# Kernel optimization log

Measured on AMD Instinct MI355X. Metric: run time of the kernel, lower is better.

The kernel has to match this reference:

```python
import jax, jax.numpy as jnp
import numpy as np

B, N, E = 2, 16384, 262144          # batch, nodes, directed edges (avg deg 16)
K, D, Wm = 256, 3, 1                # nmodes, ndims, nmeasures
C, L, FC = 128, 4, 128              # channels, Fourier layers, fc hidden
IN_DIM, OUT_DIM = 3, 1


def setup_inputs() -> dict:
    key = jax.random.key(0)
    ks = jax.random.split(key, 20)
    s = 1.0 / (C * C)
    inp = {
        "x": jax.random.normal(ks[0], (B, N, IN_DIM), jnp.float32),
        "nodes": jax.random.uniform(ks[1], (B, N, D), jnp.float32),
        "node_mask": jnp.ones((B, N, 1), jnp.float32),
        "node_weights": jax.random.uniform(ks[2], (B, N, Wm), jnp.float32) / N,
        "directed_edges": jax.random.randint(ks[3], (B, E, 2), 0, N),
        "edge_gradient_weights": jax.random.normal(ks[4], (B, E, D), jnp.float32),
        "modes": jax.random.normal(ks[5], (K, D, Wm), jnp.float32),
        "sp_L": jnp.ones((D, Wm), jnp.float32),
        "weights_c": s * jax.random.uniform(ks[6], (L, C, C, K, Wm), jnp.float32),
        "weights_s": s * jax.random.uniform(ks[7], (L, C, C, K, Wm), jnp.float32),
        "weights_0": s * jax.random.uniform(ks[8], (L, C, C, 1, Wm), jnp.float32),
        "fc0_w": jax.random.normal(ks[9], (C, IN_DIM), jnp.float32) * 0.1,
        "fc0_b": jnp.zeros((C,), jnp.float32),
        "ws_w": jax.random.normal(ks[10], (L, C, C), jnp.float32) * 0.05,
        "ws_b": jnp.zeros((L, C), jnp.float32),
        "gws_w": jax.random.normal(ks[11], (L, C, D * C), jnp.float32) * 0.05,
        "gws_b": jnp.zeros((L, C), jnp.float32),
        "fc1_w": jax.random.normal(ks[12], (FC, C), jnp.float32) * 0.05,
        "fc1_b": jnp.zeros((FC,), jnp.float32),
        "fc2_w": jax.random.normal(ks[13], (OUT_DIM, FC), jnp.float32) * 0.05,
        "fc2_b": jnp.zeros((OUT_DIM,), jnp.float32),
    }
    return inp


def _gelu(x):
    return jax.nn.gelu(x, approximate=False)  # torch F.gelu default = exact erf


def _compute_gradient(f, directed_edges, edge_gradient_weights):
    # f: [B, C, N] -> gradients [B, C*D, N] via directed-edge scatter-add
    fT = jnp.transpose(f, (0, 2, 1))                       # [B, N, C]
    tgt, src = directed_edges[..., 0], directed_edges[..., 1]
    f_src = jnp.take_along_axis(fT, src[..., None], axis=1)  # [B, E, C]
    f_tgt = jnp.take_along_axis(fT, tgt[..., None], axis=1)
    msg = jnp.einsum('bed,bec->becd', edge_gradient_weights, f_src - f_tgt)
    msg = msg.reshape(msg.shape[0], msg.shape[1], -1)        # [B, E, C*D]

    def scat(m, t):
        return jnp.zeros((fT.shape[1], m.shape[-1]), m.dtype).at[t].add(m)

    g = jax.vmap(scat)(msg, tgt)                             # [B, N, C*D]
    return jnp.transpose(g, (0, 2, 1))


def _spectral_conv(x, wc, wsn, w0, bc, bs, b0, wbc, wbs, wb0):
    # x: [B, C_in, N]
    xc = jnp.einsum('bix,bxkw->bikw', x, wbc)
    xs = -jnp.einsum('bix,bxkw->bikw', x, wbs)
    x0 = jnp.einsum('bix,bxkw->bikw', x, wb0)
    fc = jnp.einsum('bikw,iokw->bokw', xc, wc) - jnp.einsum('bikw,iokw->bokw', xs, wsn)
    fs = jnp.einsum('bikw,iokw->bokw', xs, wc) + jnp.einsum('bikw,iokw->bokw', xc, wsn)
    f0 = jnp.einsum('bikw,iokw->bokw', x0, w0)
    return (jnp.einsum('bokw,bxkw->box', f0, b0)
            + 2.0 * jnp.einsum('bokw,bxkw->box', fc, bc)
            - 2.0 * jnp.einsum('bokw,bxkw->box', fs, bs))


def reference(x, nodes, node_mask, node_weights, directed_edges, edge_gradient_weights,
              modes, sp_L, weights_c, weights_s, weights_0,
              fc0_w, fc0_b, ws_w, ws_b, gws_w, gws_b, fc1_w, fc1_b, fc2_w, fc2_b):
    # Fourier bases with learnable length-scale sp_L: [K,D,Wm]*[D,Wm]
    temp = jnp.einsum('bxd,kdw->bxkw', nodes, modes * sp_L)   # [B,N,K,Wm]
    bc, bs = jnp.cos(temp), jnp.sin(temp)
    b0 = jnp.zeros((temp.shape[0], temp.shape[1], 1, temp.shape[3]), temp.dtype)
    nw = (node_weights * node_mask)[:, :, None, :]            # [B,N,1,Wm]
    wbc, wbs, wb0 = bc * nw, bs * nw, b0 * nw

    h = jnp.einsum('bxi,ci->bxc', x, fc0_w) + fc0_b           # lift [B,N,C]
    h = jnp.transpose(h, (0, 2, 1))                           # [B,C,N]

    for i in range(L):
        x1 = _spectral_conv(h, weights_c[i], weights_s[i], weights_0[i],
                            bc, bs, b0, wbc, wbs, wb0)
        x2 = jnp.einsum('oc,bcn->bon', ws_w[i], h) + ws_b[i][None, :, None]
        grad = _compute_gradient(h, directed_edges, edge_gradient_weights)
        x3 = jnp.einsum('og,bgn->bon', gws_w[i], grad) + gws_b[i][None, :, None]
        h = x1 + x2 + x3
        if i != L - 1:
            h = _gelu(h)

    h = jnp.transpose(h, (0, 2, 1))                           # [B,N,C]
    h = _gelu(jnp.einsum('bnc,fc->bnf', h, fc1_w) + fc1_b)
    out = jnp.einsum('bnf,of->bno', h, fc2_w) + fc2_b         # [B,N,out_dim]
    return out
```

## Files before the change

### kernel.cpp

```cpp
#include <hip/hip_runtime.h>
#include <math.h>

#define Bn 2
#define Nn 16384
#define En 262144
#define Kn 256
#define Cn 128
#define Rn 512
#define Ln 4
#define LDP 72
#define NSPLIT 64

typedef float f32x4 __attribute__((ext_vector_type(4)));
typedef short s16x8 __attribute__((ext_vector_type(8)));

__device__ __forceinline__ float gelu_f(float x){
  return 0.5f*x*(1.0f + erff(x*0.70710678118654752440f));
}
__device__ __forceinline__ unsigned short f2b(float x){
  unsigned int u = __float_as_uint(x);
  unsigned int r = (u + 0x7FFFu + ((u>>16)&1u)) >> 16;
  return (unsigned short)r;
}
__device__ __forceinline__ float b2f(unsigned short h){
  return __uint_as_float(((unsigned int)h)<<16);
}
__device__ __forceinline__ unsigned int pack2(float lo, float hi){
  return (unsigned int)f2b(lo) | ((unsigned int)f2b(hi) << 16);
}


__global__ __launch_bounds__(256) void k_nw(const float* __restrict__ nwt,
                                            const float* __restrict__ msk,
                                            float* __restrict__ nw){
  int i = blockIdx.x*256 + threadIdx.x;
  nw[i] = nwt[i]*msk[i];
}

__global__ __launch_bounds__(256) void k_basis(const float* __restrict__ nodes,
                                               const float* __restrict__ modes,
                                               const float* __restrict__ spl,
                                               unsigned short* __restrict__ basis,
                                               unsigned short* __restrict__ basisT){
  __shared__ unsigned short tile[32*520];
  int gn0 = blockIdx.x*32;
  int tid = threadIdx.x;
  float m0 = modes[tid*3+0]*spl[0];
  float m1 = modes[tid*3+1]*spl[1];
  float m2 = modes[tid*3+2]*spl[2];
  for (int j=0;j<32;j++){
    const float* nd = nodes + (size_t)(gn0+j)*3;
    float t = nd[0]*m0 + nd[1]*m1 + nd[2]*m2;
    float s,c;
    sincosf(t,&s,&c);
    tile[j*520 + tid]       = f2b(c);
    tile[j*520 + 256 + tid] = f2b(s);
  }
  __syncthreads();
  int row = tid>>3, col0 = (tid&7)*64;
  #pragma unroll
  for (int q=0;q<8;q++){
    s16x8 v = *(const s16x8*)&tile[row*520 + col0 + q*8];
    *(s16x8*)(basis + (size_t)(gn0+row)*Rn + col0 + q*8) = v;
  }
  int b = gn0 >> 14;
  int nl = gn0 & (Nn-1);
  #pragma unroll
  for (int h=0; h<2; h++){
    int r = h*256 + tid;
    unsigned short* dst = basisT + ((size_t)(b*Rn + r))*Nn + nl;
    #pragma unroll
    for (int q=0;q<4;q++){
      unsigned short tmp[8];
      #pragma unroll
      for (int e=0;e<8;e++) tmp[e] = tile[(q*8+e)*520 + r];
      *(s16x8*)(dst + q*8) = *(const s16x8*)tmp;
    }
  }
}

__global__ __launch_bounds__(256) void k_lift(const float* __restrict__ x,
                                              const float* __restrict__ w,
                                              const float* __restrict__ bias,
                                              const float* __restrict__ nw,
                                              unsigned short* __restrict__ hpack,
                                              unsigned short* __restrict__ hwT){
  __shared__ float ht[64*132];
  int gn0 = blockIdx.x*64;
  int tid = threadIdx.x;
  int c = tid & 127, rh = tid >> 7;
  float w0 = w[c*3], w1 = w[c*3+1], w2 = w[c*3+2], bb = bias[c];
  for (int j=0;j<32;j++){
    int n = rh*32 + j;
    const float* xp = x + (size_t)(gn0+n)*3;
    float v = bb + xp[0]*w0 + xp[1]*w1 + xp[2]*w2;
    ht[n*132 + c] = v;
    hpack[(size_t)(gn0+n)*Cn + c] = f2b(v);
  }
  __syncthreads();
  int b = gn0 >> 14, nl = gn0 & (Nn-1);
  int cc = tid>>1, hf = tid&1;
  unsigned short* dst = hwT + ((size_t)(b*Cn + cc))*Nn + nl + hf*32;
  #pragma unroll
  for (int q=0;q<8;q++){
    int n = hf*32 + q*4;
    float4 nv = *(const float4*)&nw[(size_t)b*Nn + nl + n];
    ushort4 pk;
    pk.x = f2b(ht[(n+0)*132+cc]*nv.x);
    pk.y = f2b(ht[(n+1)*132+cc]*nv.y);
    pk.z = f2b(ht[(n+2)*132+cc]*nv.z);
    pk.w = f2b(ht[(n+3)*132+cc]*nv.w);
    *(ushort4*)(dst + q*4) = pk;
  }
}

__global__ __launch_bounds__(128) void k_w2c(const float* __restrict__ ws_w,
                                             const float* __restrict__ ws_b,
                                             const float* __restrict__ gws_w,
                                             const float* __restrict__ gws_b,
                                             unsigned short* __restrict__ W2,
                                             float* __restrict__ bias2){
  int bid = blockIdx.x;
  int tid = threadIdx.x;
  unsigned short* wrow = W2 + (size_t)bid*Rn;
  wrow[tid] = f2b(ws_w[(size_t)bid*Cn + tid]);
  const float* g = gws_w + (size_t)bid*384;
  wrow[128+tid] = f2b(g[tid*3+0]);
  wrow[256+tid] = f2b(g[tid*3+1]);
  wrow[384+tid] = f2b(g[tid*3+2]);
  if (tid==0) bias2[bid] = ws_b[bid] + gws_b[bid];
}

__global__ __launch_bounds__(256) void k_cvt(const float* __restrict__ in,
                                             unsigned short* __restrict__ out, int n){
  int i = blockIdx.x*256 + threadIdx.x;
  if (i < n) out[i] = f2b(in[i]);
}


__global__ __launch_bounds__(256) void k_count(const int* __restrict__ de,
                                               int* __restrict__ cnt){
  int i = blockIdx.x*256 + threadIdx.x;
  int b = i >> 18;
  int tgt = de[(size_t)i*2];
  atomicAdd(&cnt[b*Nn + tgt], 1);
}

__global__ __launch_bounds__(1024) void k_scan(const int* __restrict__ cnt,
                                               int* __restrict__ rowptr,
                                               int* __restrict__ cursor){
  __shared__ int part[1024];
  int t = threadIdx.x;
  int b = t >> 9;
  int li = t & 511;
  int loc[32];
  int s = 0;
  int base = b*Nn + li*32;
  #pragma unroll
  for (int j=0;j<32;j++){ loc[j] = s; s += cnt[base+j]; }
  part[t] = s;
  __syncthreads();
  int run = s;
  for (int off=1; off<512; off<<=1){
    int v = (li >= off) ? part[t-off] : 0;
    __syncthreads();
    part[t] += v;
    __syncthreads();
  }
  int incl = part[t];
  int excl = incl - run;
  int rbase = b*(Nn+1) + li*32;
  #pragma unroll
  for (int j=0;j<32;j++){
    int val = excl + loc[j];
    rowptr[rbase+j] = val;
    cursor[base+j]  = val;
  }
  if (li == 511) rowptr[b*(Nn+1) + Nn] = incl;
}

__global__ __launch_bounds__(256) void k_fill(const int* __restrict__ de,
                                              const float* __restrict__ egw,
                                              int* __restrict__ cursor,
                                              float4* __restrict__ epack){
  int i = blockIdx.x*256 + threadIdx.x;
  int b = i >> 18;
  int tgt = de[(size_t)i*2];
  int src = de[(size_t)i*2+1];
  int pos = atomicAdd(&cursor[b*Nn + tgt], 1);
  const float* g = egw + (size_t)i*3;
  float4 pk;
  pk.x = __int_as_float(src);
  pk.y = g[0]; pk.z = g[1]; pk.w = g[2];
  epack[(size_t)b*En + pos] = pk;
}

__global__ __launch_bounds__(128) void k_grad(const unsigned short* __restrict__ hpack,
                                              const float4* __restrict__ epack,
                                              const int* __restrict__ rowptr,
                                              unsigned short* __restrict__ gradbuf){
  int bid = blockIdx.x;
  int b = bid >> 14, n = bid & (Nn-1);
  int tid = threadIdx.x;
  int wv = tid >> 6;
  int l  = tid & 63;
  const unsigned short* hb = hpack + (size_t)b*Nn*Cn;
  unsigned int ft2 = *(const unsigned int*)(hb + (size_t)n*Cn + 2*l);
  float ftlo = b2f((unsigned short)(ft2 & 0xffffu));
  float fthi = b2f((unsigned short)(ft2 >> 16));
  int beg = rowptr[b*(Nn+1) + n];
  int end = rowptr[b*(Nn+1) + n + 1];
  const float4* ep = epack + (size_t)b*En;
  float a0lo=0.f,a0hi=0.f,a1lo=0.f,a1hi=0.f,a2lo=0.f,a2hi=0.f;
  int j = beg + wv;
  for (; j + 2 < end; j += 4){
    float4 pk0 = ep[j];
    float4 pk1 = ep[j+2];
    int s0 = __float_as_int(pk0.x);
    int s1 = __float_as_int(pk1.x);
    unsigned int h0 = *(const unsigned int*)(hb + (size_t)s0*Cn + 2*l);
    unsigned int h1 = *(const unsigned int*)(hb + (size_t)s1*Cn + 2*l);
    float d0lo = b2f((unsigned short)(h0 & 0xffffu)) - ftlo;
    float d0hi = b2f((unsigned short)(h0 >> 16))     - fthi;
    float d1lo = b2f((unsigned short)(h1 & 0xffffu)) - ftlo;
    float d1hi = b2f((unsigned short)(h1 >> 16))     - fthi;
    a0lo += pk0.y*d0lo + pk1.y*d1lo;  a0hi += pk0.y*d0hi + pk1.y*d1hi;
    a1lo += pk0.z*d0lo + pk1.z*d1lo;  a1hi += pk0.z*d0hi + pk1.z*d1hi;
    a2lo += pk0.w*d0lo + pk1.w*d1lo;  a2hi += pk0.w*d0hi + pk1.w*d1hi;
  }
  if (j < end){
    float4 pk = ep[j];
    int src = __float_as_int(pk.x);
    unsigned int hv = *(const unsigned int*)(hb + (size_t)src*Cn + 2*l);
    float dlo = b2f((unsigned short)(hv & 0xffffu)) - ftlo;
    float dhi = b2f((unsigned short)(hv >> 16))     - fthi;
    a0lo += pk.y*dlo; a0hi += pk.y*dhi;
    a1lo += pk.z*dlo; a1hi += pk.z*dhi;
    a2lo += pk.w*dlo; a2hi += pk.w*dhi;
  }
  __shared__ float red[64*7];
  if (wv == 1){
    float* r = &red[l*7];
    r[0]=a0lo; r[1]=a0hi; r[2]=a1lo; r[3]=a1hi; r[4]=a2lo; r[5]=a2hi;
  }
  __syncthreads();
  if (wv == 0){
    const float* r = &red[l*7];
    a0lo+=r[0]; a0hi+=r[1]; a1lo+=r[2]; a1hi+=r[3]; a2lo+=r[4]; a2hi+=r[5];
    unsigned short* o = gradbuf + ((size_t)b*Nn + n)*384;
    *(unsigned int*)(o + 2*l)       = pack2(a0lo, a0hi);
    *(unsigned int*)(o + 128 + 2*l) = pack2(a1lo, a1hi);
    *(unsigned int*)(o + 256 + 2*l) = pack2(a2lo, a2hi);
  }
}

__device__ __forceinline__ void stage_tile(const unsigned short* __restrict__ g, size_t ldg,
                                           unsigned short* __restrict__ lds, int tid){
  int row = tid >> 3;
  int seg = (tid & 7) * 8;
  #pragma unroll
  for (int rb=0; rb<4; rb++){
    s16x8 v = *(const s16x8*)(g + (size_t)(row + rb*32)*ldg + seg);
    *(s16x8*)(lds + (size_t)(row + rb*32)*LDP + seg) = v;
  }
}
__device__ __forceinline__ void stage_tile512(const unsigned short* __restrict__ g, size_t ldg,
                                              unsigned short* __restrict__ lds, int tid){
  int row = tid >> 3;
  int seg = (tid & 7) * 8;
  #pragma unroll
  for (int rb=0; rb<2; rb++){
    s16x8 v = *(const s16x8*)(g + (size_t)(row + rb*64)*ldg + seg);
    *(s16x8*)(lds + (size_t)(row + rb*64)*LDP + seg) = v;
  }
}
__device__ __forceinline__ void stage_F(const float* __restrict__ Fp, int b, int k0,
                                        unsigned short* __restrict__ lds, int tid){
  int row = tid >> 3;
  int col0 = (tid & 7) * 8;
  float sc = (k0 < 256) ? 2.f : -2.f;
  #pragma unroll
  for (int rb=0; rb<2; rb++){
    int r = row + rb*64;
    const float* p0 = Fp + ((size_t)b*Cn + r)*Rn + k0 + col0;
    const float* p1 = p0 + (size_t)Bn*Cn*Rn;
    f32x4 a0 = *(const f32x4*)p0;
    f32x4 a1 = *(const f32x4*)(p0+4);
    f32x4 c0 = *(const f32x4*)p1;
    f32x4 c1 = *(const f32x4*)(p1+4);
    unsigned short tmp[8];
    #pragma unroll
    for (int e=0;e<4;e++){
      tmp[e]   = f2b((a0[e]+c0[e])*sc);
      tmp[4+e] = f2b((a1[e]+c1[e])*sc);
    }
    *(s16x8*)(lds + (size_t)r*LDP + col0) = *(const s16x8*)tmp;
  }
}

__device__ __forceinline__ void mfma_chunk(const unsigned short* __restrict__ As,
                                           const unsigned short* __restrict__ Bs,
                                           f32x4 acc[4][4], int wm, int wn, int lr, int lg){
  #pragma unroll
  for (int kk=0; kk<2; kk++){
    s16x8 a[4], b[4];
    #pragma unroll
    for (int i=0;i<4;i++)
      a[i] = *(const s16x8*)(As + (size_t)(wm*64 + i*16 + lr)*LDP + kk*32 + lg*8);
    #pragma unroll
    for (int i=0;i<4;i++)
      b[i] = *(const s16x8*)(Bs + (size_t)(wn*64 + i*16 + lr)*LDP + kk*32 + lg*8);
    #pragma unroll
    for (int i=0;i<4;i++)
      #pragma unroll
      for (int j=0;j<4;j++)
        acc[i][j] = __builtin_amdgcn_mfma_f32_16x16x32_bf16(a[i], b[j], acc[i][j], 0, 0, 0);
  }
}

__device__ __forceinline__ void mfma_chunk8(const unsigned short* __restrict__ As,
                                            const unsigned short* __restrict__ Bs,
                                            f32x4 acc[4][2], int wm, int wn, int lr, int lg){
  #pragma unroll
  for (int kk=0; kk<2; kk++){
    s16x8 a[4], b[2];
    #pragma unroll
    for (int i=0;i<4;i++)
      a[i] = *(const s16x8*)(As + (size_t)(wm*64 + i*16 + lr)*LDP + kk*32 + lg*8);
    #pragma unroll
    for (int j=0;j<2;j++)
      b[j] = *(const s16x8*)(Bs + (size_t)(wn*32 + j*16 + lr)*LDP + kk*32 + lg*8);
    #pragma unroll
    for (int i=0;i<4;i++)
      #pragma unroll
      for (int j=0;j<2;j++)
        acc[i][j] = __builtin_amdgcn_mfma_f32_16x16x32_bf16(a[i], b[j], acc[i][j], 0, 0, 0);
  }
}

__global__ __launch_bounds__(256) void k_fwd_mfma(const unsigned short* __restrict__ basisT,
                                                  const unsigned short* __restrict__ hwT,
                                                  float* __restrict__ part){
  __shared__ unsigned short As[128*LDP];
  __shared__ unsigned short Bs[128*LDP];
  int tid = threadIdx.x;
  int mt = blockIdx.x;
  int ks = blockIdx.y;
  int b  = blockIdx.z;
  const int KSP = Nn/NSPLIT;
  const unsigned short* A  = basisT + ((size_t)(b*Rn + mt*128))*Nn + (size_t)ks*KSP;
  const unsigned short* Bp = hwT   + ((size_t)(b*Cn))*Nn + (size_t)ks*KSP;
  f32x4 acc[4][4] = {};
  int l = tid & 63, w = tid >> 6, wm = w >> 1, wn = w & 1, lr = l & 15, lg = l >> 4;
  for (int k0 = 0; k0 < KSP; k0 += 64){
    stage_tile(A + k0, Nn, As, tid);
    stage_tile(Bp + k0, Nn, Bs, tid);
    __syncthreads();
    mfma_chunk(As, Bs, acc, wm, wn, lr, lg);
    __syncthreads();
  }
  float* pb = part + ((size_t)ks*Bn + b)*(Cn*Rn);
  int r0 = mt*128 + wm*64;
  int c0 = wn*64;
  #pragma unroll
  for (int i=0;i<4;i++)
    #pragma unroll
    for (int j=0;j<4;j++){
      int r = r0 + i*16 + lg*4;
      int c = c0 + j*16 + lr;
      *(f32x4*)&pb[(size_t)c*Rn + r] = acc[i][j];
    }
}

__global__ __launch_bounds__(256) void k_reduce(const float* __restrict__ part,
                                                float* __restrict__ xf){
  int idx = blockIdx.x*256 + threadIdx.x;
  float s = 0.f;
  #pragma unroll 8
  for (int ks=0; ks<NSPLIT; ks++)
    s += part[(size_t)ks*(Bn*Cn*Rn) + idx];
  xf[idx] = s;
}

__global__ __launch_bounds__(512) void k_mm(const float* __restrict__ xf,
                                            const float* __restrict__ wc,
                                            const float* __restrict__ ws,
                                            float* __restrict__ Fpart){
  int o  = blockIdx.x;
  int is = blockIdx.y;
  int tid = threadIdx.x;
  int half = tid >> 8, t = tid & 255;
  int ibase = is*64 + half*32;
  float fc0=0.f, fs0=0.f, fc1=0.f, fs1=0.f;
  for (int ii=0; ii<32; ii++){
    int i = ibase + ii;
    float wcv = wc[((size_t)i*Cn + o)*Kn + t];
    float wsv = ws[((size_t)i*Cn + o)*Kn + t];
    float x0c = xf[(size_t)i*Rn + t];
    float x0s = xf[(size_t)i*Rn + 256 + t];
    float x1c = xf[(size_t)Cn*Rn + (size_t)i*Rn + t];
    float x1s = xf[(size_t)Cn*Rn + (size_t)i*Rn + 256 + t];
    fc0 += x0c*wcv + x0s*wsv;  fs0 += x0c*wsv - x0s*wcv;
    fc1 += x1c*wcv + x1s*wsv;  fs1 += x1c*wsv - x1s*wcv;
  }
  __shared__ float red[4][256];
  if (half){ red[0][t]=fc0; red[1][t]=fs0; red[2][t]=fc1; red[3][t]=fs1; }
  __syncthreads();
  if (!half){
    fc0 += red[0][t]; fs0 += red[1][t];
    fc1 += red[2][t]; fs1 += red[3][t];
    float* f0 = Fpart + ((size_t)(is*Bn + 0)*Cn + o)*Rn;
    float* f1 = Fpart + ((size_t)(is*Bn + 1)*Cn + o)*Rn;
    f0[t]     = fc0;  f0[256+t] = fs0;
    f1[t]     = fc1;  f1[256+t] = fs1;
  }
}

template<int GELU, int WRITE_AUX>
__global__ __launch_bounds__(512) void k_invcomb(const unsigned short* __restrict__ basis,
                                                 const float* __restrict__ Fpart,
                                                 const unsigned short* __restrict__ gradbuf,
                                                 const unsigned short* __restrict__ W2l,
                                                 const float* __restrict__ bias2l,
                                                 const float* __restrict__ nw,
                                                 unsigned short* __restrict__ hpack,
                                                 unsigned short* __restrict__ hwT){
  __shared__ unsigned short As1[128*LDP];
  __shared__ unsigned short Bs1[128*LDP];
  __shared__ unsigned short As2[128*LDP];
  __shared__ unsigned short Bs2[128*LDP];
  int tid = threadIdx.x;
  int nt = blockIdx.x;
  int b  = blockIdx.y;
  size_t nbase = (size_t)b*Nn + (size_t)nt*128;
  f32x4 acc[4][2] = {};
  int l = tid & 63, w = tid >> 6, wm = w >> 2, wn = w & 3, lr = l & 15, lg = l >> 4;
  const unsigned short* A1 = basis + nbase*Rn;
  for (int k0=0;k0<512;k0+=64){
    stage_tile512(A1+k0, Rn, As1, tid);
    stage_F(Fpart, b, k0, Bs1, tid);
    if (k0 < 128) stage_tile512(hpack + nbase*Cn + k0, Cn, As2, tid);
    else          stage_tile512(gradbuf + nbase*384 + (k0-128), 384, As2, tid);
    stage_tile512(W2l+k0, Rn, Bs2, tid);
    __syncthreads();
    mfma_chunk8(As1,Bs1,acc,wm,wn,lr,lg);
    mfma_chunk8(As2,Bs2,acc,wm,wn,lr,lg);
    __syncthreads();
  }
  #pragma unroll
  for (int i=0;i<4;i++){
    int nloc = wm*64 + i*16 + lg*4;
    float4 w4;
    if (WRITE_AUX) w4 = *(const float4*)&nw[(size_t)b*Nn + nt*128 + nloc];
    #pragma unroll
    for (int j=0;j<2;j++){
      int c = wn*32 + j*16 + lr;
      float bsv = bias2l[c];
      float v[4];
      #pragma unroll
      for (int e=0;e<4;e++){
        v[e] = acc[i][j][e] + bsv;
        if (GELU) v[e] = gelu_f(v[e]);
        hpack[(nbase + nloc + e)*Cn + c] = f2b(v[e]);
      }
      if (WRITE_AUX){
        ushort4 pk;
        pk.x = f2b(v[0]*w4.x); pk.y = f2b(v[1]*w4.y);
        pk.z = f2b(v[2]*w4.z); pk.w = f2b(v[3]*w4.w);
        *(ushort4*)&hwT[((size_t)(b*Cn + c))*Nn + nt*128 + nloc] = pk;
      }
    }
  }
}

__global__ __launch_bounds__(512) void k_fc1(const unsigned short* __restrict__ hpack,
                                             const unsigned short* __restrict__ fw,
                                             const float* __restrict__ fb,
                                             unsigned short* __restrict__ h2){
  __shared__ unsigned short As[128*LDP];
  __shared__ unsigned short Bs[128*LDP];
  int tid = threadIdx.x;
  int nt = blockIdx.x;
  int b  = blockIdx.y;
  size_t nbase = (size_t)b*Nn + (size_t)nt*128;
  f32x4 acc[4][2] = {};
  int l = tid & 63, w = tid >> 6, wm = w >> 2, wn = w & 3, lr = l & 15, lg = l >> 4;
  const unsigned short* A = hpack + nbase*Cn;
  for (int k0=0;k0<128;k0+=64){
    stage_tile512(A+k0, Cn, As, tid);
    stage_tile512(fw+k0, Cn, Bs, tid);
    __syncthreads();
    mfma_chunk8(As,Bs,acc,wm,wn,lr,lg);
    __syncthreads();
  }
  #pragma unroll
  for (int i=0;i<4;i++){
    int nloc = wm*64 + i*16 + lg*4;
    #pragma unroll
    for (int j=0;j<2;j++){
      int c = wn*32 + j*16 + lr;
      float bsv = fb[c];
      #pragma unroll
      for (int e=0;e<4;e++){
        float v = gelu_f(acc[i][j][e] + bsv);
        h2[(nbase + nloc + e)*Cn + c] = f2b(v);
      }
    }
  }
}

__global__ __launch_bounds__(256) void k_out(const unsigned short* __restrict__ h2,
                                             const float* __restrict__ w,
                                             const float* __restrict__ bptr,
                                             float* __restrict__ outp){
  int tid = threadIdx.x;
  int node = blockIdx.x*4 + (tid>>6);
  int f = tid & 63;
  const unsigned short* hp = h2 + (size_t)node*Cn;
  float s = b2f(hp[f])*w[f] + b2f(hp[f+64])*w[f+64];
  #pragma unroll
  for (int off=32; off>0; off>>=1) s += __shfl_down(s, off);
  if (f==0) outp[node] = s + bptr[0];
}

static constexpr size_t OB_BASIS  = 0;
static constexpr size_t OB_BASIST = OB_BASIS  + 33554432;
static constexpr size_t OB_GRAD   = OB_BASIST + 33554432;
static constexpr size_t OB_HWT    = OB_GRAD   + 25165824;
static constexpr size_t OB_H2     = OB_HWT    + 8388608;
static constexpr size_t OB_HP     = OB_H2     + 8388608;
static constexpr size_t OB_NW     = OB_HP     + 8388608;
static constexpr size_t OB_XF     = OB_NW     + 131072;
static constexpr size_t OB_FPART  = OB_XF     + 524288;
static constexpr size_t OB_W2     = OB_FPART  + 1048576;
static constexpr size_t OB_B2     = OB_W2     + 524288;
static constexpr size_t OB_FC1W   = OB_B2     + 2048;
static constexpr size_t OB_EPACK  = OB_FC1W   + 32768;
static constexpr size_t OB_INT    = OB_EPACK  + 8388608;
static constexpr size_t OB_PART   = OB_INT    + 524288;

extern "C" void kernel_launch(void* const* d_in, const int* in_sizes, int n_in,
                              void* d_out, int out_size, void* d_ws, size_t ws_size,
                              hipStream_t stream) {
  const float* x            = (const float*)d_in[0];
  const float* nodes        = (const float*)d_in[1];
  const float* node_mask    = (const float*)d_in[2];
  const float* node_weights = (const float*)d_in[3];
  const int*   de           = (const int*)  d_in[4];
  const float* egw          = (const float*)d_in[5];
  const float* modes        = (const float*)d_in[6];
  const float* spl          = (const float*)d_in[7];
  const float* wc           = (const float*)d_in[8];
  const float* wsp          = (const float*)d_in[9];
  const float* fc0_w        = (const float*)d_in[11];
  const float* fc0_b        = (const float*)d_in[12];
  const float* ws_w         = (const float*)d_in[13];
  const float* ws_b         = (const float*)d_in[14];
  const float* gws_w        = (const float*)d_in[15];
  const float* gws_b        = (const float*)d_in[16];
  const float* fc1_w        = (const float*)d_in[17];
  const float* fc1_b        = (const float*)d_in[18];
  const float* fc2_w        = (const float*)d_in[19];
  const float* fc2_b        = (const float*)d_in[20];
  float* outp = (float*)d_out;

  char* wsb = (char*)d_ws;
  unsigned short* basis   = (unsigned short*)(wsb + OB_BASIS);
  unsigned short* basisT  = (unsigned short*)(wsb + OB_BASIST);
  unsigned short* gradbuf = (unsigned short*)(wsb + OB_GRAD);
  unsigned short* hwT     = (unsigned short*)(wsb + OB_HWT);
  unsigned short* h2      = (unsigned short*)(wsb + OB_H2);
  unsigned short* hpack   = (unsigned short*)(wsb + OB_HP);
  float* nw               = (float*)(wsb + OB_NW);
  float* xf               = (float*)(wsb + OB_XF);
  float* Fpart            = (float*)(wsb + OB_FPART);
  unsigned short* W2      = (unsigned short*)(wsb + OB_W2);
  float* bias2            = (float*)(wsb + OB_B2);
  unsigned short* fc1wb   = (unsigned short*)(wsb + OB_FC1W);
  float4* epack           = (float4*)(wsb + OB_EPACK);
  int* count  = (int*)(wsb + OB_INT);
  int* rowptr = count + Bn*Nn;
  int* cursor = rowptr + Bn*(Nn+1);
  float* part = (float*)(wsb + OB_PART);

  k_nw<<<(Bn*Nn)/256, 256, 0, stream>>>(node_weights, node_mask, nw);
  k_basis<<<(Bn*Nn)/32, 256, 0, stream>>>(nodes, modes, spl, basis, basisT);
  k_lift<<<(Bn*Nn)/64, 256, 0, stream>>>(x, fc0_w, fc0_b, nw, hpack, hwT);

  (void)hipMemsetAsync(count, 0, (size_t)Bn*Nn*sizeof(int), stream);
  k_count<<<(Bn*En)/256, 256, 0, stream>>>(de, count);
  k_scan<<<1, 1024, 0, stream>>>(count, rowptr, cursor);
  k_fill<<<(Bn*En)/256, 256, 0, stream>>>(de, egw, cursor, epack);

  k_w2c<<<Ln*Cn, 128, 0, stream>>>(ws_w, ws_b, gws_w, gws_b, W2, bias2);
  k_cvt<<<64, 256, 0, stream>>>(fc1_w, fc1wb, Cn*Cn);

  for (int l=0; l<Ln; l++){
    k_fwd_mfma<<<dim3(4,NSPLIT,2), 256, 0, stream>>>(basisT, hwT, part);
    k_reduce<<<(Bn*Cn*Rn)/256, 256, 0, stream>>>(part, xf);
    k_mm<<<dim3(Cn,2), 512, 0, stream>>>(xf, wc + (size_t)l*Cn*Cn*Kn,
                                         wsp + (size_t)l*Cn*Cn*Kn, Fpart);
    k_grad<<<Bn*Nn, 128, 0, stream>>>(hpack, epack, rowptr, gradbuf);
    if (l < Ln-1){
      k_invcomb<1,1><<<dim3(Nn/128,2), 512, 0, stream>>>(
          basis, Fpart, gradbuf, W2 + (size_t)l*Cn*Rn, bias2 + l*Cn, nw, hpack, hwT);
    } else {
      k_invcomb<0,0><<<dim3(Nn/128,2), 512, 0, stream>>>(
          basis, Fpart, gradbuf, W2 + (size_t)l*Cn*Rn, bias2 + l*Cn, nw, hpack, hwT);
    }
  }

  k_fc1<<<dim3(Nn/128,2), 512, 0, stream>>>(hpack, fc1wb, fc1_b, h2);
  k_out<<<(Bn*Nn)/4, 256, 0, stream>>>(h2, fc2_w, fc2_b, outp);
}
```

Before: 534.4 us.

## Read GEMM B operands from global memory, pre-convert F to bf16, widen k_grad

```diff
diff --git a/kernel.cpp b/kernel.cpp
--- a/kernel.cpp
+++ b/kernel.cpp
@@ -195,7 +195,7 @@
   epack[(size_t)b*En + pos] = pk;
 }
 
-__global__ __launch_bounds__(128) void k_grad(const unsigned short* __restrict__ hpack,
+__global__ __launch_bounds__(256) void k_grad(const unsigned short* __restrict__ hpack,
                                               const float4* __restrict__ epack,
                                               const int* __restrict__ rowptr,
                                               unsigned short* __restrict__ gradbuf){
@@ -213,9 +213,9 @@
   const float4* ep = epack + (size_t)b*En;
   float a0lo=0.f,a0hi=0.f,a1lo=0.f,a1hi=0.f,a2lo=0.f,a2hi=0.f;
   int j = beg + wv;
-  for (; j + 2 < end; j += 4){
+  for (; j + 4 < end; j += 8){
     float4 pk0 = ep[j];
-    float4 pk1 = ep[j+2];
+    float4 pk1 = ep[j+4];
     int s0 = __float_as_int(pk0.x);
     int s1 = __float_as_int(pk1.x);
     unsigned int h0 = *(const unsigned int*)(hb + (size_t)s0*Cn + 2*l);
@@ -238,15 +238,18 @@
     a1lo += pk.z*dlo; a1hi += pk.z*dhi;
     a2lo += pk.w*dlo; a2hi += pk.w*dhi;
   }
-  __shared__ float red[64*7];
-  if (wv == 1){
-    float* r = &red[l*7];
+  __shared__ float red[3][64*6];
+  if (wv > 0){
+    float* r = &red[wv-1][l*6];
     r[0]=a0lo; r[1]=a0hi; r[2]=a1lo; r[3]=a1hi; r[4]=a2lo; r[5]=a2hi;
   }
   __syncthreads();
   if (wv == 0){
-    const float* r = &red[l*7];
-    a0lo+=r[0]; a0hi+=r[1]; a1lo+=r[2]; a1hi+=r[3]; a2lo+=r[4]; a2hi+=r[5];
+    #pragma unroll
+    for (int q=0;q<3;q++){
+      const float* r = &red[q][l*6];
+      a0lo+=r[0]; a0hi+=r[1]; a1lo+=r[2]; a1hi+=r[3]; a2lo+=r[4]; a2hi+=r[5];
+    }
     unsigned short* o = gradbuf + ((size_t)b*Nn + n)*384;
     *(unsigned int*)(o + 2*l)       = pack2(a0lo, a0hi);
     *(unsigned int*)(o + 128 + 2*l) = pack2(a1lo, a1hi);
@@ -274,33 +277,10 @@
     *(s16x8*)(lds + (size_t)(row + rb*64)*LDP + seg) = v;
   }
 }
-__device__ __forceinline__ void stage_F(const float* __restrict__ Fp, int b, int k0,
-                                        unsigned short* __restrict__ lds, int tid){
-  int row = tid >> 3;
-  int col0 = (tid & 7) * 8;
-  float sc = (k0 < 256) ? 2.f : -2.f;
-  #pragma unroll
-  for (int rb=0; rb<2; rb++){
-    int r = row + rb*64;
-    const float* p0 = Fp + ((size_t)b*Cn + r)*Rn + k0 + col0;
-    const float* p1 = p0 + (size_t)Bn*Cn*Rn;
-    f32x4 a0 = *(const f32x4*)p0;
-    f32x4 a1 = *(const f32x4*)(p0+4);
-    f32x4 c0 = *(const f32x4*)p1;
-    f32x4 c1 = *(const f32x4*)(p1+4);
-    unsigned short tmp[8];
-    #pragma unroll
-    for (int e=0;e<4;e++){
-      tmp[e]   = f2b((a0[e]+c0[e])*sc);
-      tmp[4+e] = f2b((a1[e]+c1[e])*sc);
-    }
-    *(s16x8*)(lds + (size_t)r*LDP + col0) = *(const s16x8*)tmp;
-  }
-}
-
-__device__ __forceinline__ void mfma_chunk(const unsigned short* __restrict__ As,
-                                           const unsigned short* __restrict__ Bs,
-                                           f32x4 acc[4][4], int wm, int wn, int lr, int lg){
+
+__device__ __forceinline__ void mfma_gb4(const unsigned short* __restrict__ As,
+                                         const unsigned short* __restrict__ Bg, size_t ldb,
+                                         f32x4 acc[4][4], int wm, int wn, int lr, int lg){
   #pragma unroll
   for (int kk=0; kk<2; kk++){
     s16x8 a[4], b[4];
@@ -308,8 +288,8 @@
     for (int i=0;i<4;i++)
       a[i] = *(const s16x8*)(As + (size_t)(wm*64 + i*16 + lr)*LDP + kk*32 + lg*8);
     #pragma unroll
-    for (int i=0;i<4;i++)
-      b[i] = *(const s16x8*)(Bs + (size_t)(wn*64 + i*16 + lr)*LDP + kk*32 + lg*8);
+    for (int j=0;j<4;j++)
+      b[j] = *(const s16x8*)(Bg + (size_t)(wn*64 + j*16 + lr)*ldb + kk*32 + lg*8);
     #pragma unroll
     for (int i=0;i<4;i++)
       #pragma unroll
@@ -318,9 +298,9 @@
   }
 }
 
-__device__ __forceinline__ void mfma_chunk8(const unsigned short* __restrict__ As,
-                                            const unsigned short* __restrict__ Bs,
-                                            f32x4 acc[4][2], int wm, int wn, int lr, int lg){
+__device__ __forceinline__ void mfma_gb8(const unsigned short* __restrict__ As,
+                                         const unsigned short* __restrict__ Bg, size_t ldb,
+                                         f32x4 acc[4][2], int wm, int wn, int lr, int lg){
   #pragma unroll
   for (int kk=0; kk<2; kk++){
     s16x8 a[4], b[2];
@@ -329,7 +309,7 @@
       a[i] = *(const s16x8*)(As + (size_t)(wm*64 + i*16 + lr)*LDP + kk*32 + lg*8);
     #pragma unroll
     for (int j=0;j<2;j++)
-      b[j] = *(const s16x8*)(Bs + (size_t)(wn*32 + j*16 + lr)*LDP + kk*32 + lg*8);
+      b[j] = *(const s16x8*)(Bg + (size_t)(wn*32 + j*16 + lr)*ldb + kk*32 + lg*8);
     #pragma unroll
     for (int i=0;i<4;i++)
       #pragma unroll
@@ -342,7 +322,6 @@
                                                   const unsigned short* __restrict__ hwT,
                                                   float* __restrict__ part){
   __shared__ unsigned short As[128*LDP];
-  __shared__ unsigned short Bs[128*LDP];
   int tid = threadIdx.x;
   int mt = blockIdx.x;
   int ks = blockIdx.y;
@@ -354,9 +333,8 @@
   int l = tid & 63, w = tid >> 6, wm = w >> 1, wn = w & 1, lr = l & 15, lg = l >> 4;
   for (int k0 = 0; k0 < KSP; k0 += 64){
     stage_tile(A + k0, Nn, As, tid);
-    stage_tile(Bp + k0, Nn, Bs, tid);
-    __syncthreads();
-    mfma_chunk(As, Bs, acc, wm, wn, lr, lg);
+    __syncthreads();
+    mfma_gb4(As, Bp + k0, Nn, acc, wm, wn, lr, lg);
     __syncthreads();
   }
   float* pb = part + ((size_t)ks*Bn + b)*(Cn*Rn);
@@ -416,9 +394,17 @@
   }
 }
 
+__global__ __launch_bounds__(256) void k_fcvt(const float* __restrict__ Fpart,
+                                              unsigned short* __restrict__ Fbf){
+  int idx = blockIdx.x*256 + threadIdx.x;
+  float s = Fpart[idx] + Fpart[idx + Bn*Cn*Rn];
+  float sc = ((idx & 511) < 256) ? 2.f : -2.f;
+  Fbf[idx] = f2b(sc*s);
+}
+
 template<int GELU, int WRITE_AUX>
 __global__ __launch_bounds__(512) void k_invcomb(const unsigned short* __restrict__ basis,
-                                                 const float* __restrict__ Fpart,
+                                                 const unsigned short* __restrict__ Fbf,
                                                  const unsigned short* __restrict__ gradbuf,
                                                  const unsigned short* __restrict__ W2l,
                                                  const float* __restrict__ bias2l,
@@ -426,9 +412,7 @@
                                                  unsigned short* __restrict__ hpack,
                                                  unsigned short* __restrict__ hwT){
   __shared__ unsigned short As1[128*LDP];
-  __shared__ unsigned short Bs1[128*LDP];
   __shared__ unsigned short As2[128*LDP];
-  __shared__ unsigned short Bs2[128*LDP];
   int tid = threadIdx.x;
   int nt = blockIdx.x;
   int b  = blockIdx.y;
@@ -436,15 +420,14 @@
   f32x4 acc[4][2] = {};
   int l = tid & 63, w = tid >> 6, wm = w >> 2, wn = w & 3, lr = l & 15, lg = l >> 4;
   const unsigned short* A1 = basis + nbase*Rn;
+  const unsigned short* B1 = Fbf + (size_t)b*Cn*Rn;
   for (int k0=0;k0<512;k0+=64){
     stage_tile512(A1+k0, Rn, As1, tid);
-    stage_F(Fpart, b, k0, Bs1, tid);
     if (k0 < 128) stage_tile512(hpack + nbase*Cn + k0, Cn, As2, tid);
     else          stage_tile512(gradbuf + nbase*384 + (k0-128), 384, As2, tid);
-    stage_tile512(W2l+k0, Rn, Bs2, tid);
-    __syncthreads();
-    mfma_chunk8(As1,Bs1,acc,wm,wn,lr,lg);
-    mfma_chunk8(As2,Bs2,acc,wm,wn,lr,lg);
+    __syncthreads();
+    mfma_gb8(As1, B1 + k0, Rn, acc, wm, wn, lr, lg);
+    mfma_gb8(As2, W2l + k0, Rn, acc, wm, wn, lr, lg);
     __syncthreads();
   }
   #pragma unroll
@@ -478,7 +461,6 @@
                                              const float* __restrict__ fb,
                                              unsigned short* __restrict__ h2){
   __shared__ unsigned short As[128*LDP];
-  __shared__ unsigned short Bs[128*LDP];
   int tid = threadIdx.x;
   int nt = blockIdx.x;
   int b  = blockIdx.y;
@@ -488,9 +470,8 @@
   const unsigned short* A = hpack + nbase*Cn;
   for (int k0=0;k0<128;k0+=64){
     stage_tile512(A+k0, Cn, As, tid);
-    stage_tile512(fw+k0, Cn, Bs, tid);
-    __syncthreads();
-    mfma_chunk8(As,Bs,acc,wm,wn,lr,lg);
+    __syncthreads();
+    mfma_gb8(As, fw + k0, Cn, acc, wm, wn, lr, lg);
     __syncthreads();
   }
   #pragma unroll
@@ -531,7 +512,8 @@
 static constexpr size_t OB_HP     = OB_H2     + 8388608;
 static constexpr size_t OB_NW     = OB_HP     + 8388608;
 static constexpr size_t OB_XF     = OB_NW     + 131072;
-static constexpr size_t OB_FPART  = OB_XF     + 524288;
+static constexpr size_t OB_FBF    = OB_XF     + 524288;
+static constexpr size_t OB_FPART  = OB_FBF    + 262144;
 static constexpr size_t OB_W2     = OB_FPART  + 1048576;
 static constexpr size_t OB_B2     = OB_W2     + 524288;
 static constexpr size_t OB_FC1W   = OB_B2     + 2048;
@@ -573,6 +555,7 @@
   unsigned short* hpack   = (unsigned short*)(wsb + OB_HP);
   float* nw               = (float*)(wsb + OB_NW);
   float* xf               = (float*)(wsb + OB_XF);
+  unsigned short* Fbf     = (unsigned short*)(wsb + OB_FBF);
   float* Fpart            = (float*)(wsb + OB_FPART);
   unsigned short* W2      = (unsigned short*)(wsb + OB_W2);
   float* bias2            = (float*)(wsb + OB_B2);
@@ -600,13 +583,14 @@
     k_reduce<<<(Bn*Cn*Rn)/256, 256, 0, stream>>>(part, xf);
     k_mm<<<dim3(Cn,2), 512, 0, stream>>>(xf, wc + (size_t)l*Cn*Cn*Kn,
                                          wsp + (size_t)l*Cn*Cn*Kn, Fpart);
-    k_grad<<<Bn*Nn, 128, 0, stream>>>(hpack, epack, rowptr, gradbuf);
+    k_fcvt<<<(Bn*Cn*Rn)/256, 256, 0, stream>>>(Fpart, Fbf);
+    k_grad<<<Bn*Nn, 256, 0, stream>>>(hpack, epack, rowptr, gradbuf);
     if (l < Ln-1){
       k_invcomb<1,1><<<dim3(Nn/128,2), 512, 0, stream>>>(
-          basis, Fpart, gradbuf, W2 + (size_t)l*Cn*Rn, bias2 + l*Cn, nw, hpack, hwT);
+          basis, Fbf, gradbuf, W2 + (size_t)l*Cn*Rn, bias2 + l*Cn, nw, hpack, hwT);
     } else {
       k_invcomb<0,0><<<dim3(Nn/128,2), 512, 0, stream>>>(
-          basis, Fpart, gradbuf, W2 + (size_t)l*Cn*Rn, bias2 + l*Cn, nw, hpack, hwT);
+          basis, Fbf, gradbuf, W2 + (size_t)l*Cn*Rn, bias2 + l*Cn, nw, hpack, hwT);
     }
   }
 
```

After: 602.0 us. +12.6%, slower.
